# Kernel tuning notes

Hardware: AMD Instinct MI355X
Metric: run time of the kernel (lower is better)

## Reference

```python
import jax, jax.numpy as jnp
import numpy as np

B, CIN, COUT, H, W, KK = 1, 32, 64, 181, 360, 4
NNZ_PER, NNZ_PER1 = 9, 4


def _make_psi(rng, K, H, W, nnz_per):
    # Sparse DISCO basis in COO form for longitude 0 (shift-invariant in lon).
    E = K * H * nnz_per
    seg = np.repeat(np.arange(K * H, dtype=np.int32), nnz_per)  # k*H + ho
    ho = seg % H
    dlat = rng.integers(-1, 2, size=E).astype(np.int32)
    hi = np.clip(ho + dlat, 0, H - 1).astype(np.int32)
    wi = (rng.integers(-1, 2, size=E).astype(np.int32)) % W
    vals = (rng.normal(size=E) * 0.2).astype(np.float32)
    return seg, hi, wi, vals


def setup_inputs() -> dict:
    rng = np.random.default_rng(0)
    key = jax.random.key(0)
    ks = jax.random.split(key, 5)
    x = jax.random.normal(ks[0], (B, CIN, H, W), dtype=jnp.float32)
    # spherical quadrature weights: sin(colatitude) * cell area
    theta = np.linspace(0.0, np.pi, H)
    qw = (np.sin(theta) * (np.pi / (H - 1)) * (2.0 * np.pi / W)).astype(np.float32)
    qw = np.maximum(qw, 1e-8).reshape(H, 1)
    seg, hi, wi, vals = _make_psi(rng, KK, H, W, NNZ_PER)
    seg1, hi1, wi1, vals1 = _make_psi(rng, 1, H, W, NNZ_PER1)
    w_depth = jax.random.normal(ks[1], (CIN, KK), dtype=jnp.float32) / np.sqrt(KK)
    w_point = jax.random.normal(ks[2], (COUT, CIN), dtype=jnp.float32) / np.sqrt(CIN)
    bias = jax.random.normal(ks[3], (COUT,), dtype=jnp.float32) * 0.02
    return {
        "x": x,
        "quad_w": jnp.asarray(qw),
        "vals": jnp.asarray(vals),
        "seg": jnp.asarray(seg),
        "hi": jnp.asarray(hi),
        "wi": jnp.asarray(wi),
        "w_depth": w_depth,
        "vals1": jnp.asarray(vals1),
        "seg1": jnp.asarray(seg1),
        "hi1": jnp.asarray(hi1),
        "wi1": jnp.asarray(wi1),
        "w_point": w_point,
        "bias": bias,
        "K": KK,
    }


def _disco_contract(x, vals, seg, hi, wi, K):
    # x: [B,C,H,W]; COO psi at lon 0; out[b,c,k,ho,wo] =
    #   sum_{e: seg[e]==k*H+ho} vals[e] * x[b,c,hi[e],(wi[e]+wo) mod W]
    Bq, C, Hq, Wq = x.shape
    rows = x[:, :, hi, :]                                        # [B,C,E,W]
    col = (wi[:, None] + jnp.arange(Wq, dtype=wi.dtype)[None, :]) % Wq  # [E,W]
    rolled = jnp.take_along_axis(rows, col[None, None, :, :], axis=3)   # [B,C,E,W]
    weighted = rolled * vals[None, None, :, None]
    out = jax.ops.segment_sum(weighted.transpose(2, 0, 1, 3), seg,
                              num_segments=K * Hq)               # [K*H,B,C,W]
    return out.reshape(K, Hq, Bq, C, Wq).transpose(2, 3, 0, 1, 4)  # [B,C,K,H,W]


def reference(x, quad_w, vals, seg, hi, wi, w_depth, vals1, seg1, hi1, wi1,
              w_point, bias, K):
    # depthwise DISCO conv (groups=C_in, no bias)
    xq = x * quad_w                                   # quadrature weighting
    xd = _disco_contract(xq, vals, seg, hi, wi, K)    # [B,C,K,H,W]
    y = jnp.einsum("ck,bckhw->bchw", w_depth, xd)     # per-channel K mix
    # pointwise DISCO conv (kernel_shape=1) = CLinear
    yq = y * quad_w
    z = _disco_contract(yq, vals1, seg1, hi1, wi1, 1)[:, :, 0]  # [B,C,H,W]
    out = jnp.einsum("oc,bchw->bohw", w_point, z) + bias[None, :, None, None]
    return out
```

## Files before the change

### kernel.cpp

```cpp
#include <hip/hip_runtime.h>


#define H_    181
#define W_    360
#define CIN_  32
#define COUT_ 64
#define K_    4
#define NNZ_  9
#define NNZ1_ 4
#define HW_   (H_*W_)
#define NT_   (NNZ1_*K_*NNZ_)
#define HWPB_ 180
#define TPB_  256
#define ZP_   33
#define NLOG_ 362

__global__ __launch_bounds__(TPB_) void sepconv_fused(
    const float* __restrict__ x, const float* __restrict__ quad_w,
    const float* __restrict__ vals, const int* __restrict__ hi,
    const int* __restrict__ wi, const float* __restrict__ w_depth,
    const float* __restrict__ vals1, const int* __restrict__ hi1,
    const int* __restrict__ wi1, const float* __restrict__ w_point,
    const float* __restrict__ bias, float* __restrict__ out)
{
    const int bid = blockIdx.x;
    const int L   = (bid & 7) * 46 + (bid >> 3);
    if (L >= NLOG_) return;
    const int h    = L >> 1;
    const int half = L & 1;
    const int tid  = threadIdx.x;

    __shared__ float Tval[NT_];
    __shared__ int   Tbin[NT_];
    __shared__ float S[K_][25];
    __shared__ float C[CIN_][25];
    __shared__ float zsm[HWPB_ * ZP_];

    if (tid < NT_) {
        const int a   = tid / 36;
        const int rem = tid - a * 36;
        const int k   = rem / 9;
        const int j   = rem - k * 9;
        const int e1  = h * NNZ1_ + a;
        const int m   = hi1[e1];
        const int w1  = wi1[e1];
        const int d1  = (w1 == 1) ? 1 : ((w1 == 0) ? 0 : -1);
        const int e   = (k * H_ + m) * NNZ_ + j;
        const int r   = hi[e];
        const int w0  = wi[e];
        const int d   = (w0 == 1) ? 1 : ((w0 == 0) ? 0 : -1);
        Tval[tid] = vals1[e1] * quad_w[m] * vals[e] * quad_w[r];
        Tbin[tid] = (r - h + 2) * 5 + (d1 + d + 2);
    }
    __syncthreads();

    if (tid < K_ * 25) {
        const int k   = tid / 25;
        const int bin = tid - k * 25;
        float s = 0.f;
        #pragma unroll
        for (int a = 0; a < NNZ1_; ++a)
            #pragma unroll
            for (int j = 0; j < NNZ_; ++j) {
                const int t2 = a * 36 + k * 9 + j;
                if (Tbin[t2] == bin) s += Tval[t2];
            }
        S[k][bin] = s;
    }
    __syncthreads();

    for (int item = tid; item < CIN_ * 25; item += TPB_) {
        const int c   = item / 25;
        const int bin = item - c * 25;
        float acc = 0.f;
        #pragma unroll
        for (int k = 0; k < K_; ++k) acc += w_depth[c * K_ + k] * S[k][bin];
        C[c][bin] = acc;
    }
    __syncthreads();

    if (tid < HWPB_) {
        const int chg = tid & 3;
        const int pg  = tid >> 2;
        const int bw  = half * HWPB_ + pg * 4;
        const int cA  = (bw + W_ - 4) % W_;
        const int cB  = bw;
        const int cC  = (bw + 4) % W_;

        int rowoff[5];
        #pragma unroll
        for (int rb = 0; rb < 5; ++rb) {
            int r = h - 2 + rb;
            r = (r < 0) ? 0 : ((r > H_ - 1) ? H_ - 1 : r);
            rowoff[rb] = r * W_;
        }

        #pragma unroll 2
        for (int cc = 0; cc < 8; ++cc) {
            const int c = chg * 8 + cc;
            const float* xc = x + c * HW_;
            const float* Cc = &C[c][0];
            float a0 = 0.f, a1 = 0.f, a2 = 0.f, a3 = 0.f;
            #pragma unroll
            for (int rb = 0; rb < 5; ++rb) {
                const float* xr = xc + rowoff[rb];
                const float4 vA = *(const float4*)(xr + cA);
                const float4 vB = *(const float4*)(xr + cB);
                const float4 vC = *(const float4*)(xr + cC);
                const float k0 = Cc[rb * 5 + 0], k1 = Cc[rb * 5 + 1],
                            k2 = Cc[rb * 5 + 2], k3 = Cc[rb * 5 + 3],
                            k4 = Cc[rb * 5 + 4];
                a0 += k0 * vA.z + k1 * vA.w + k2 * vB.x + k3 * vB.y + k4 * vB.z;
                a1 += k0 * vA.w + k1 * vB.x + k2 * vB.y + k3 * vB.z + k4 * vB.w;
                a2 += k0 * vB.x + k1 * vB.y + k2 * vB.z + k3 * vB.w + k4 * vC.x;
                a3 += k0 * vB.y + k1 * vB.z + k2 * vB.w + k3 * vC.x + k4 * vC.y;
            }
            const int p0 = pg * 4;
            zsm[(p0 + 0) * ZP_ + c] = a0;
            zsm[(p0 + 1) * ZP_ + c] = a1;
            zsm[(p0 + 2) * ZP_ + c] = a2;
            zsm[(p0 + 3) * ZP_ + c] = a3;
        }
    }
    __syncthreads();

    if (tid < HWPB_) {
        float z[CIN_];
        #pragma unroll
        for (int c = 0; c < CIN_; ++c) z[c] = zsm[tid * ZP_ + c];

        const int w = half * HWPB_ + tid;
        float* op = out + h * W_ + w;
        #pragma unroll 4
        for (int o = 0; o < COUT_; ++o) {
            float acc = bias[o];
            #pragma unroll
            for (int c = 0; c < CIN_; ++c) acc += w_point[o * CIN_ + c] * z[c];
            op[o * HW_] = acc;
        }
    }
}

extern "C" void kernel_launch(void* const* d_in, const int* in_sizes, int n_in,
                              void* d_out, int out_size, void* d_ws, size_t ws_size,
                              hipStream_t stream) {
    const float* x       = (const float*)d_in[0];
    const float* quad_w  = (const float*)d_in[1];
    const float* vals    = (const float*)d_in[2];
    const int*   hi      = (const int*)d_in[4];
    const int*   wi      = (const int*)d_in[5];
    const float* w_depth = (const float*)d_in[6];
    const float* vals1   = (const float*)d_in[7];
    const int*   hi1     = (const int*)d_in[9];
    const int*   wi1     = (const int*)d_in[10];
    const float* w_point = (const float*)d_in[11];
    const float* bias    = (const float*)d_in[12];

    sepconv_fused<<<368, TPB_, 0, stream>>>(
        x, quad_w, vals, hi, wi, w_depth, vals1, hi1, wi1,
        w_point, bias, (float*)d_out);
}
```

Baseline: 135.8 us.

## Split fused kernel into stencil and pointwise kernels via workspace

Splits the single fused kernel into a stencil kernel that writes the depthwise result z to a global workspace, and a separate pointwise kernel that does the 64x32 channel mix. The stencil grid is split across channel segments (184x8 blocks) and the pointwise kernel tiles 128 pixels per block with all 256 threads active, aiming to raise parallelism and occupancy over the old 368-block launch where only 180 of 256 threads worked. In exchange, z makes a round trip through global memory (about 8 MB written and read) and there is a second launch.

```diff
diff --git a/kernel.cpp b/kernel.cpp
--- a/kernel.cpp
+++ b/kernel.cpp
@@ -10,31 +10,25 @@
 #define NNZ1_ 4
 #define HW_   (H_*W_)
 #define NT_   (NNZ1_*K_*NNZ_)
-#define HWPB_ 180
-#define TPB_  256
-#define ZP_   33
-#define NLOG_ 362
+#define PXT_  128
 
-__global__ __launch_bounds__(TPB_) void sepconv_fused(
+__global__ __launch_bounds__(256) void sepconv_stencil(
     const float* __restrict__ x, const float* __restrict__ quad_w,
     const float* __restrict__ vals, const int* __restrict__ hi,
     const int* __restrict__ wi, const float* __restrict__ w_depth,
     const float* __restrict__ vals1, const int* __restrict__ hi1,
-    const int* __restrict__ wi1, const float* __restrict__ w_point,
-    const float* __restrict__ bias, float* __restrict__ out)
+    const int* __restrict__ wi1, float* __restrict__ z)
 {
-    const int bid = blockIdx.x;
-    const int L   = (bid & 7) * 46 + (bid >> 3);
-    if (L >= NLOG_) return;
-    const int h    = L >> 1;
-    const int half = L & 1;
+    const int bx = blockIdx.x;
+    const int h  = (bx & 7) * 23 + (bx >> 3);
+    if (h >= H_) return;
+    const int cseg = blockIdx.y;
     const int tid  = threadIdx.x;
 
     __shared__ float Tval[NT_];
     __shared__ int   Tbin[NT_];
     __shared__ float S[K_][25];
-    __shared__ float C[CIN_][25];
-    __shared__ float zsm[HWPB_ * ZP_];
+    __shared__ float C[4][25];
 
     if (tid < NT_) {
         const int a   = tid / 36;
@@ -69,74 +63,89 @@
     }
     __syncthreads();
 
-    for (int item = tid; item < CIN_ * 25; item += TPB_) {
-        const int c   = item / 25;
-        const int bin = item - c * 25;
+    if (tid < 4 * 25) {
+        const int c4  = tid / 25;
+        const int bin = tid - c4 * 25;
+        const int c   = cseg * 4 + c4;
         float acc = 0.f;
         #pragma unroll
         for (int k = 0; k < K_; ++k) acc += w_depth[c * K_ + k] * S[k][bin];
-        C[c][bin] = acc;
+        C[c4][bin] = acc;
     }
     __syncthreads();
 
-    if (tid < HWPB_) {
-        const int chg = tid & 3;
-        const int pg  = tid >> 2;
-        const int bw  = half * HWPB_ + pg * 4;
-        const int cA  = (bw + W_ - 4) % W_;
-        const int cB  = bw;
-        const int cC  = (bw + 4) % W_;
+    int rowoff[5];
+    #pragma unroll
+    for (int rb = 0; rb < 5; ++rb) {
+        int r = h - 2 + rb;
+        r = (r < 0) ? 0 : ((r > H_ - 1) ? H_ - 1 : r);
+        rowoff[rb] = r * W_;
+    }
 
-        int rowoff[5];
+    for (int item = tid; item < 4 * 90; item += 256) {
+        const int c4 = item / 90;
+        const int g  = item - c4 * 90;
+        const int c  = cseg * 4 + c4;
+        const int bw = g * 4;
+        const int cA = (bw + W_ - 4) % W_;
+        const int cB = bw;
+        const int cC = (bw + 4) % W_;
+        const float* xc = x + c * HW_;
+        const float* Cc = &C[c4][0];
+
+        float a0 = 0.f, a1 = 0.f, a2 = 0.f, a3 = 0.f;
         #pragma unroll
         for (int rb = 0; rb < 5; ++rb) {
-            int r = h - 2 + rb;
-            r = (r < 0) ? 0 : ((r > H_ - 1) ? H_ - 1 : r);
-            rowoff[rb] = r * W_;
+            const float* xr = xc + rowoff[rb];
+            const float4 vA = *(const float4*)(xr + cA);
+            const float4 vB = *(const float4*)(xr + cB);
+            const float4 vC = *(const float4*)(xr + cC);
+            const float k0 = Cc[rb * 5 + 0], k1 = Cc[rb * 5 + 1],
+                        k2 = Cc[rb * 5 + 2], k3 = Cc[rb * 5 + 3],
+                        k4 = Cc[rb * 5 + 4];
+            a0 += k0 * vA.z + k1 * vA.w + k2 * vB.x + k3 * vB.y + k4 * vB.z;
+            a1 += k0 * vA.w + k1 * vB.x + k2 * vB.y + k3 * vB.z + k4 * vB.w;
+            a2 += k0 * vB.x + k1 * vB.y + k2 * vB.z + k3 * vB.w + k4 * vC.x;
+            a3 += k0 * vB.y + k1 * vB.z + k2 * vB.w + k3 * vC.x + k4 * vC.y;
         }
+        float4 r4; r4.x = a0; r4.y = a1; r4.z = a2; r4.w = a3;
+        *(float4*)(z + c * HW_ + h * W_ + bw) = r4;
+    }
+}
 
-        #pragma unroll 2
-        for (int cc = 0; cc < 8; ++cc) {
-            const int c = chg * 8 + cc;
-            const float* xc = x + c * HW_;
-            const float* Cc = &C[c][0];
-            float a0 = 0.f, a1 = 0.f, a2 = 0.f, a3 = 0.f;
-            #pragma unroll
-            for (int rb = 0; rb < 5; ++rb) {
-                const float* xr = xc + rowoff[rb];
-                const float4 vA = *(const float4*)(xr + cA);
-                const float4 vB = *(const float4*)(xr + cB);
-                const float4 vC = *(const float4*)(xr + cC);
-                const float k0 = Cc[rb * 5 + 0], k1 = Cc[rb * 5 + 1],
-                            k2 = Cc[rb * 5 + 2], k3 = Cc[rb * 5 + 3],
-                            k4 = Cc[rb * 5 + 4];
-                a0 += k0 * vA.z + k1 * vA.w + k2 * vB.x + k3 * vB.y + k4 * vB.z;
-                a1 += k0 * vA.w + k1 * vB.x + k2 * vB.y + k3 * vB.z + k4 * vB.w;
-                a2 += k0 * vB.x + k1 * vB.y + k2 * vB.z + k3 * vB.w + k4 * vC.x;
-                a3 += k0 * vB.y + k1 * vB.z + k2 * vB.w + k3 * vC.x + k4 * vC.y;
-            }
-            const int p0 = pg * 4;
-            zsm[(p0 + 0) * ZP_ + c] = a0;
-            zsm[(p0 + 1) * ZP_ + c] = a1;
-            zsm[(p0 + 2) * ZP_ + c] = a2;
-            zsm[(p0 + 3) * ZP_ + c] = a3;
-        }
+__global__ __launch_bounds__(256) void sepconv_pointwise(
+    const float* __restrict__ z, const float* __restrict__ w_point,
+    const float* __restrict__ bias, float* __restrict__ out)
+{
+    const int p0  = blockIdx.x * PXT_;
+    const int tid = threadIdx.x;
+
+    __shared__ float zs[CIN_][PXT_];
+    for (int i = tid; i < CIN_ * PXT_; i += 256) {
+        const int c = i >> 7;
+        const int j = i & (PXT_ - 1);
+        const int p = p0 + j;
+        zs[c][j] = (p < HW_) ? z[c * HW_ + p] : 0.f;
     }
     __syncthreads();
 
-    if (tid < HWPB_) {
-        float z[CIN_];
-        #pragma unroll
-        for (int c = 0; c < CIN_; ++c) z[c] = zsm[tid * ZP_ + c];
+    const int j  = tid & (PXT_ - 1);
+    const int oh = tid >> 7;
+    const int p  = p0 + j;
 
-        const int w = half * HWPB_ + tid;
-        float* op = out + h * W_ + w;
-        #pragma unroll 4
-        for (int o = 0; o < COUT_; ++o) {
-            float acc = bias[o];
+    float zr[CIN_];
+    #pragma unroll
+    for (int c = 0; c < CIN_; ++c) zr[c] = zs[c][j];
+
+    if (p < HW_) {
+        const float* wp = w_point + oh * 32 * CIN_;
+        float* op = out + oh * 32 * HW_ + p;
+        #pragma unroll 8
+        for (int oo = 0; oo < 32; ++oo) {
+            float acc = bias[oh * 32 + oo];
             #pragma unroll
-            for (int c = 0; c < CIN_; ++c) acc += w_point[o * CIN_ + c] * z[c];
-            op[o * HW_] = acc;
+            for (int c = 0; c < CIN_; ++c) acc += wp[oo * CIN_ + c] * zr[c];
+            op[oo * HW_] = acc;
         }
     }
 }
@@ -156,7 +165,10 @@
     const float* w_point = (const float*)d_in[11];
     const float* bias    = (const float*)d_in[12];
 
-    sepconv_fused<<<368, TPB_, 0, stream>>>(
-        x, quad_w, vals, hi, wi, w_depth, vals1, hi1, wi1,
-        w_point, bias, (float*)d_out);
+    float* z = (float*)d_ws;
+
+    sepconv_stencil<<<dim3(184, 8), 256, 0, stream>>>(
+        x, quad_w, vals, hi, wi, w_depth, vals1, hi1, wi1, z);
+    sepconv_pointwise<<<(HW_ + PXT_ - 1) / PXT_, 256, 0, stream>>>(
+        z, w_point, bias, (float*)d_out);
 }
```

Measured after the change: 125.7 us. 1.08x faster.
